# Kernel tuning notes

Hardware: AMD Instinct MI355X
Metric: run time of the kernel (lower is better)

The kernel has to match this reference:

```python
import jax, jax.numpy as jnp
import numpy as np

N_NODES, N_EDGES = 16000, 256000
M_IN_S, M_IN_V = 16, 8   # input irreps: 16x0e + 8x1o (dim 40)
M_K_S, M_K_V = 8, 4      # key/query irreps: 8x0e + 4x1o
M_V_S, M_V_V = 16, 8     # value irreps: 16x0e + 8x1o
NUM_BASIS, R_CUT = 32, 2.5
SQ3 = 1.7320508075688772  # sqrt(3)


def _fc_net(r, W1, W2):
    # e3nn FullyConnectedNet([num_basis,16,numels], silu): weight-normalized linears
    h = jax.nn.silu(r @ (W1 / jnp.sqrt(jnp.float32(W1.shape[0]))))
    return h @ (W2 / jnp.sqrt(jnp.float32(W2.shape[0])))


def _edge_tp(xs, xv, y0, y1, w, m1s, m1v, mos, mov):
    # FullyConnectedTensorProduct(in1 = m1s x0e + m1v x1o, in2 = 1x0e + 1x1o,
    #   out = mos x0e + mov x1o), per-edge external weights w [E, numels].
    # Paths: 0e*0e->0e, 1o*1o->0e (dot/sqrt3), 0e*1o->1o, 1o*0e->1o.
    E = w.shape[0]
    n1, n2, n3 = m1s * mos, m1v * mos, m1s * mov
    w_ss = w[:, :n1].reshape(E, m1s, mos)
    w_vv = w[:, n1:n1 + n2].reshape(E, m1v, mos)
    w_sv = w[:, n1 + n2:n1 + n2 + n3].reshape(E, m1s, mov)
    w_vs = w[:, n1 + n2 + n3:].reshape(E, m1v, mov)
    inv = 1.0 / jnp.sqrt(jnp.float32(m1s + m1v))  # fan-in path normalization
    out_s = (jnp.einsum('ei,eio->eo', xs * y0[:, None], w_ss)
             + jnp.einsum('eic,ec,eio->eo', xv, y1, w_vv) / SQ3) * inv
    out_v = (jnp.einsum('ei,ec,eio->eoc', xs, y1, w_sv)
             + jnp.einsum('eic,eio->eoc', xv * y0[:, None, None], w_vs)) * inv
    return out_s, out_v


def _forward(pos, x, Wq_s, Wq_v, Wk1, Wk2, Wv1, Wv2, Ws_ss, Ws_vv, edge_src, edge_dst):
    xs, xv = x[:, :M_IN_S], x[:, M_IN_S:].reshape(-1, M_IN_V, 3)
    vec = pos[edge_dst] - pos[edge_src]                       # [E,3]
    d = jnp.linalg.norm(vec, axis=1)
    d_safe = jnp.maximum(d, 1e-6)
    # bessel radial basis with cutoff (soft_one_hot_linspace, basis='bessel') * sqrt(num_basis)
    n = jnp.arange(1, NUM_BASIS + 1, dtype=jnp.float32)
    rad = jnp.sqrt(2.0 / R_CUT) * jnp.sin(n[None] * jnp.pi * d_safe[:, None] / R_CUT) / d_safe[:, None]
    rad = jnp.where((d < R_CUT)[:, None], rad, 0.0) * jnp.sqrt(jnp.float32(NUM_BASIS))
    # spherical harmonics lmax=1, normalize=True, component normalization
    vh = vec / d_safe[:, None]
    y0, y1 = jnp.ones_like(d), SQ3 * vh
    # query projection (o3.Linear: per-irrep linear with 1/sqrt(fan_in))
    q_s = xs @ Wq_s / jnp.sqrt(jnp.float32(M_IN_S))           # [N, M_K_S]
    q_v = jnp.einsum('nic,io->noc', xv, Wq_v) / jnp.sqrt(jnp.float32(M_IN_V))
    # per-edge tensor-product weights from radial MLPs (shared_weights=False)
    wk = _fc_net(rad, Wk1, Wk2)                               # [E, 288]
    wv = _fc_net(rad, Wv1, Wv2)                               # [E, 576]
    xs_e, xv_e = xs[edge_src], xv[edge_src]
    k_s, k_v = _edge_tp(xs_e, xv_e, y0, y1, wk, M_IN_S, M_IN_V, M_K_S, M_K_V)
    v_s, v_v = _edge_tp(xs_e, xv_e, y0, y1, wv, M_IN_S, M_IN_V, M_V_S, M_V_V)
    # similarity tensor product (query x key -> 0e), shared internal weights
    fan = jnp.sqrt(jnp.float32(M_K_S * M_K_S + M_K_V * M_K_V))
    sim = (jnp.einsum('ei,ij,ej->e', q_s[edge_dst], Ws_ss, k_s)
           + jnp.einsum('eic,ij,ejc->e', q_v[edge_dst], Ws_vv, k_v) / SQ3) / fan
    # scatter softmax over incoming edges of each dst node
    attn = jnp.exp(sim)
    Z = jax.ops.segment_sum(attn, edge_dst, num_segments=N_NODES)
    a = attn / Z[edge_dst]
    # weighted scatter-sum aggregation
    out_s = jax.ops.segment_sum(a[:, None] * v_s, edge_dst, num_segments=N_NODES)
    out_v = jax.ops.segment_sum(a[:, None, None] * v_v, edge_dst, num_segments=N_NODES)
    return jnp.concatenate([out_s, out_v.reshape(N_NODES, -1)], axis=1)  # [N, 40]


def setup_inputs() -> dict:
    key = jax.random.key(0)
    ks = jax.random.split(key, 12)
    wk_numels = M_IN_S * M_K_S + M_IN_V * M_K_S + M_IN_S * M_K_V + M_IN_V * M_K_V  # 288
    wv_numels = M_IN_S * M_V_S + M_IN_V * M_V_S + M_IN_S * M_V_V + M_IN_V * M_V_V  # 576
    return {
        'pos': jax.random.uniform(ks[0], (N_NODES, 3), jnp.float32) * 3.0,
        'x': jax.random.normal(ks[1], (N_NODES, M_IN_S + 3 * M_IN_V), jnp.float32),
        'Wq_s': jax.random.normal(ks[2], (M_IN_S, M_K_S), jnp.float32),
        'Wq_v': jax.random.normal(ks[3], (M_IN_V, M_K_V), jnp.float32),
        'Wk1': jax.random.normal(ks[4], (NUM_BASIS, 16), jnp.float32),
        'Wk2': jax.random.normal(ks[5], (16, wk_numels), jnp.float32),
        'Wv1': jax.random.normal(ks[6], (NUM_BASIS, 16), jnp.float32),
        'Wv2': jax.random.normal(ks[7], (16, wv_numels), jnp.float32),
        'Ws_ss': jax.random.normal(ks[8], (M_K_S, M_K_S), jnp.float32) * 0.1,
        'Ws_vv': jax.random.normal(ks[9], (M_K_V, M_K_V), jnp.float32) * 0.1,
        'edge_src': jax.random.randint(ks[10], (N_EDGES,), 0, N_NODES),
        'edge_dst': jax.random.randint(ks[11], (N_EDGES,), 0, N_NODES),
    }


def reference(pos, x, Wq_s, Wq_v, Wk1, Wk2, Wv1, Wv2, Ws_ss, Ws_vv, edge_src, edge_dst):
    return _forward(pos, x, Wq_s, Wq_v, Wk1, Wk2, Wv1, Wv2, Ws_ss, Ws_vv, edge_src, edge_dst)
```

## Files before the change

kernel.cpp:

```cpp
#include <hip/hip_runtime.h>
#include <hip/hip_bf16.h>

#define N_NODES 16000
#define N_EDGES 256000

#define OFF_SD     0
#define OFF_SIMB   512000
#define OFF_CNT    768000
#define OFF_START  784000
#define OFF_CUR    800001
#define OFF_WB     816004
#define OFF_WBK    834436
#define OFF_QT     846724

typedef _Float16 f16x2 __attribute__((ext_vector_type(2)));
typedef _Float16 f16x8v __attribute__((ext_vector_type(8)));
typedef float f32x4v __attribute__((ext_vector_type(4)));

__device__ __forceinline__ float fdot2f(f16x2 a, f16x2 b, float c) {
#if __has_builtin(__builtin_amdgcn_fdot2)
  return __builtin_amdgcn_fdot2(a, b, c, false);
#else
  return fmaf((float)a.x, (float)b.x, fmaf((float)a.y, (float)b.y, c));
#endif
}

__device__ __forceinline__ unsigned packh2(float a, float b) {
  union { unsigned u; f16x2 p; } v;
  v.p.x = (_Float16)a; v.p.y = (_Float16)b;
  return v.u;
}

__device__ __forceinline__ unsigned splat_half(unsigned x, unsigned sel) {
#if __has_builtin(__builtin_amdgcn_perm)
  return __builtin_amdgcn_perm(x, x, sel);
#else
  unsigned h = (sel == 0x03020302u) ? (x >> 16) : (x & 0xffffu);
  return h | (h << 16);
#endif
}

__device__ __forceinline__ void load_row40(const float* __restrict__ p, float* xr) {
  const float4* rp = reinterpret_cast<const float4*>(p);
#pragma unroll
  for (int q = 0; q < 10; ++q) {
    float4 f = rp[q];
    xr[4 * q + 0] = f.x; xr[4 * q + 1] = f.y; xr[4 * q + 2] = f.z; xr[4 * q + 3] = f.w;
  }
}

struct EdgeGeom { float vhx, vhy, vhz, y1x, y1y, y1z; };

__device__ __forceinline__ void edge_h_pk(const float* __restrict__ pos, int s, int d,
                                          const unsigned* W1, f16x2* hp, EdgeGeom& g) {
  float vx = pos[3 * d + 0] - pos[3 * s + 0];
  float vy = pos[3 * d + 1] - pos[3 * s + 1];
  float vz = pos[3 * d + 2] - pos[3 * s + 2];
  float dist = sqrtf(fmaf(vx, vx, fmaf(vy, vy, vz * vz)));
  float dsafe = fmaxf(dist, 1e-6f);
  float rinv = 1.0f / dsafe;
  g.vhx = vx * rinv; g.vhy = vy * rinv; g.vhz = vz * rinv;
  g.y1x = 1.7320508075688772f * g.vhx;
  g.y1y = 1.7320508075688772f * g.vhy;
  g.y1z = 1.7320508075688772f * g.vhz;
  float pre[16];
#pragma unroll
  for (int t = 0; t < 16; ++t) pre[t] = 0.f;
  float sx, cx;
  sincosf(1.2566370614359172f * dsafe, &sx, &cx);
  cx = fminf(1.f, fmaxf(-1.f, cx));
  float twoc = 2.f * cx;
  float sprev = 0.f, scur = sx;
  float rscale = (dist < 2.5f) ? (5.059644256269407f * rinv) : 0.f;
#pragma unroll
  for (int bp = 0; bp < 16; ++bp) {
    float r0 = rscale * scur;
    float sn = fmaf(twoc, scur, -sprev); sprev = scur; scur = sn;
    float r1 = rscale * scur;
    sn = fmaf(twoc, scur, -sprev); sprev = scur; scur = sn;
    union { unsigned u; f16x2 p; } rp; rp.p.x = (_Float16)r0; rp.p.y = (_Float16)r1;
    union { uint4 u[4]; f16x2 p[16]; } w;
    w.u[0] = *(const uint4*)(W1 + bp * 16);
    w.u[1] = *(const uint4*)(W1 + bp * 16 + 4);
    w.u[2] = *(const uint4*)(W1 + bp * 16 + 8);
    w.u[3] = *(const uint4*)(W1 + bp * 16 + 12);
#pragma unroll
    for (int t = 0; t < 16; ++t) pre[t] = fdot2f(rp.p, w.p[t], pre[t]);
  }
#pragma unroll
  for (int tp = 0; tp < 8; ++tp) {
    float h0 = pre[2 * tp]     / (1.f + __expf(-pre[2 * tp]));
    float h1 = pre[2 * tp + 1] / (1.f + __expf(-pre[2 * tp + 1]));
    hp[tp].x = (_Float16)h0; hp[tp].y = (_Float16)h1;
  }
}

__global__ void k_hist(const int* __restrict__ edst, int* __restrict__ cnt) {
  int e = blockIdx.x * 256 + threadIdx.x;
  atomicAdd(&cnt[edst[e]], 1);
}

__global__ void __launch_bounds__(1024) k_scan(const int* __restrict__ cnt,
                                               int* __restrict__ start, int* __restrict__ cur) {
  __shared__ int part[1024];
  int t = threadIdx.x;
  int base = t * 16;
  int local[16];
  int sum = 0;
#pragma unroll
  for (int i = 0; i < 16; ++i) {
    int idx = base + i;
    int c = (idx < N_NODES) ? cnt[idx] : 0;
    local[i] = sum; sum += c;
  }
  part[t] = sum;
  __syncthreads();
  for (int off = 1; off < 1024; off <<= 1) {
    int v = (t >= off) ? part[t - off] : 0;
    __syncthreads();
    part[t] += v;
    __syncthreads();
  }
  int prev = (t == 0) ? 0 : part[t - 1];
#pragma unroll
  for (int i = 0; i < 16; ++i) {
    int idx = base + i;
    if (idx < N_NODES) { int st = prev + local[i]; start[idx] = st; cur[idx] = st; }
  }
  if (t == 0) start[N_NODES] = N_EDGES;
}

__global__ void k_fill(const int* __restrict__ esrc, const int* __restrict__ edst,
                       int* __restrict__ cur, int2* __restrict__ sd) {
  int e = blockIdx.x * 256 + threadIdx.x;
  int d = edst[e];
  int slot = atomicAdd(&cur[d], 1);
  sd[slot] = make_int2(esrc[e], d);
}

__global__ void k_prepB(const float* __restrict__ Wv2, unsigned short* __restrict__ WB) {
  int idx = blockIdx.x * 256 + threadIdx.x;
  int j = idx & 7;
  int lane = (idx >> 3) & 63;
  int t3 = idx >> 9;
  int ct = t3 % 3, kk = t3 / 3;
  int q = lane >> 4, m = lane & 15;
  int row = 32 * kk + 8 * q + j;
  int col = 16 * ct + m;
  int t = row & 15;
  float v = 0.f;
  if (row < 256) {
    int i = row >> 4;
    if (col < 16)      v = Wv2[t * 576 + i * 16 + col];
    else if (col < 24) v = Wv2[t * 576 + 384 + i * 8 + (col - 16)];
  } else if (row < 384) {
    int i = (row - 256) >> 4;
    if (col < 16)      v = Wv2[t * 576 + 256 + i * 16 + col];
  } else {
    int part = (row - 384) >> 7;
    int i = ((row - 384) & 127) >> 4;
    int cb = 24 + 8 * part;
    if (col >= cb && col < cb + 8) v = Wv2[t * 576 + 512 + i * 8 + (col - cb)];
  }
  union { unsigned short u; _Float16 h; } cv;
  cv.h = (_Float16)(v * 0.051031036307982884f);
  WB[idx] = cv.u;
}

__global__ void k_prepBK(const float* __restrict__ Wk2, unsigned short* __restrict__ WBK) {
  int idx = blockIdx.x * 256 + threadIdx.x;
  int j = idx & 7;
  int lane = (idx >> 3) & 63;
  int t2 = idx >> 9;
  int ct = t2 & 1, kk = t2 >> 1;
  int q = lane >> 4, m = lane & 15;
  int row = 32 * kk + 8 * q + j;
  int col = 16 * ct + m;
  int t = row & 15;
  float v = 0.f;
  if (col < 24) {
    if (row < 256) {
      int i = row >> 4;
      if (col < 8)       v = Wk2[t * 288 + i * 8 + col];
      else if (col < 12) v = Wk2[t * 288 + 192 + i * 4 + (col - 8)];
    } else if (row < 384) {
      int i = (row - 256) >> 4;
      if (col < 8)       v = Wk2[t * 288 + 128 + i * 8 + col];
    } else {
      int c = (row - 384) >> 7;
      int i = ((row - 384) & 127) >> 4;
      int cb = 12 + 4 * c;
      if (col >= cb && col < cb + 4) v = Wk2[t * 288 + 256 + i * 4 + (col - cb)];
    }
  }
  union { unsigned short u; _Float16 h; } cv;
  cv.h = (_Float16)(v * 0.051031036307982884f);
  WBK[idx] = cv.u;
}

__global__ void __launch_bounds__(128) k_nodeq(
    const float* __restrict__ x,
    const float* __restrict__ Wq_s, const float* __restrict__ Wq_v,
    const float* __restrict__ Wss, const float* __restrict__ Wvv,
    unsigned short* __restrict__ QT) {
  __shared__ float Ls[240];
  for (int i = threadIdx.x; i < 240; i += 128) {
    float v;
    if (i < 128)      v = Wq_s[i] * 0.25f;
    else if (i < 160) v = Wq_v[i - 128] * 0.3535533905932738f;
    else if (i < 224) v = Wss[i - 160] * 0.11180339887498948f;
    else              v = Wvv[i - 224] * 0.06454972243679028f;
    Ls[i] = v;
  }
  __syncthreads();
  int n = blockIdx.x * 128 + threadIdx.x;
  float xd[40];
  load_row40(x + 40 * n, xd);
  float qd[8], qvd[12];
#pragma unroll
  for (int o = 0; o < 8; ++o) qd[o] = 0.f;
#pragma unroll
  for (int i = 0; i < 16; ++i)
#pragma unroll
    for (int o = 0; o < 8; ++o) qd[o] = fmaf(xd[i], Ls[8 * i + o], qd[o]);
#pragma unroll
  for (int k = 0; k < 12; ++k) qvd[k] = 0.f;
#pragma unroll
  for (int i = 0; i < 8; ++i)
#pragma unroll
    for (int o = 0; o < 4; ++o)
#pragma unroll
      for (int c = 0; c < 3; ++c)
        qvd[3 * o + c] = fmaf(xd[16 + 3 * i + c], Ls[128 + 4 * i + o], qvd[3 * o + c]);
  float qf[20];
#pragma unroll
  for (int j = 0; j < 8; ++j) {
    float t = 0.f;
#pragma unroll
    for (int i = 0; i < 8; ++i) t = fmaf(qd[i], Ls[160 + 8 * i + j], t);
    qf[j] = t;
  }
#pragma unroll
  for (int o = 0; o < 4; ++o)
#pragma unroll
    for (int c = 0; c < 3; ++c) {
      float t = 0.f;
#pragma unroll
      for (int i = 0; i < 4; ++i) t = fmaf(qvd[3 * i + c], Ls[224 + 4 * i + o], t);
      qf[8 + 3 * o + c] = t;
    }
  uint2* qp = (uint2*)(QT + 20 * n);
#pragma unroll
  for (int b = 0; b < 5; ++b) {
    uint2 st;
    st.x = packh2(qf[4 * b], qf[4 * b + 1]);
    st.y = packh2(qf[4 * b + 2], qf[4 * b + 3]);
    qp[b] = st;
  }
}

#define RSTR 36

__device__ __forceinline__ void build_coef(const float* xr, const float* Bv, float* coef) {
#pragma unroll
  for (int i = 0; i < 16; ++i) coef[i] = xr[i];
#pragma unroll
  for (int i = 0; i < 8; ++i) coef[16 + i] = Bv[i];
#pragma unroll
  for (int p = 0; p < 4; ++p)
#pragma unroll
    for (int c = 0; c < 3; ++c) {
      coef[24 + 8 * c + 2 * p]     = xr[16 + 6 * p + c];
      coef[24 + 8 * c + 2 * p + 1] = xr[16 + 6 * p + 3 + c];
    }
}

__global__ void __launch_bounds__(256) k_edge1(
    const float* __restrict__ pos, const float* __restrict__ x,
    const float* __restrict__ Wk1, const unsigned short* __restrict__ WBK,
    const unsigned short* __restrict__ QT,
    const int2* __restrict__ sd, float* __restrict__ simb) {
  __shared__ __align__(16) unsigned LW1[256];
  __shared__ __align__(16) unsigned SM[4][64 * RSTR];

  for (int i = threadIdx.x; i < 256; i += 256) {
    int bp = i >> 4, t = i & 15;
    LW1[i] = packh2(Wk1[(2 * bp) * 16 + t] * 0.17677669529663687f,
                    Wk1[(2 * bp + 1) * 16 + t] * 0.17677669529663687f);
  }
  __syncthreads();

  int wave = threadIdx.x >> 6, lane = threadIdx.x & 63;
  int q = lane >> 4, m = lane & 15;
  int q1 = q & 1;
  unsigned seld = (q >> 1) ? 0x03020302u : 0x01000100u;
  int slot = blockIdx.x * 256 + threadIdx.x;
  int2 e = sd[slot];
  int s = e.x, d = e.y;

  f16x2 hp[8]; EdgeGeom g;
  edge_h_pk(pos, s, d, LW1, hp, g);

  float qf[20];
  {
    const uint2* qp = (const uint2*)(QT + 20 * d);
#pragma unroll
    for (int b = 0; b < 5; ++b) {
      uint2 u = qp[b];
      union { unsigned d; f16x2 p; } a0, a1;
      a0.d = u.x; a1.d = u.y;
      qf[4 * b] = (float)a0.p.x; qf[4 * b + 1] = (float)a0.p.y;
      qf[4 * b + 2] = (float)a1.p.x; qf[4 * b + 3] = (float)a1.p.y;
    }
  }

  float xr[40];
  load_row40(x + 40 * s, xr);
  float Bv[8];
#pragma unroll
  for (int i = 0; i < 8; ++i)
    Bv[i] = fmaf(xr[16 + 3 * i], g.vhx, fmaf(xr[17 + 3 * i], g.vhy, xr[18 + 3 * i] * g.vhz));
  float coef[48];
  build_coef(xr, Bv, coef);

  unsigned* row = &SM[wave][lane * RSTR];
  {
    union { uint4 u; f16x2 p[4]; } h0, h1;
#pragma unroll
    for (int k = 0; k < 4; ++k) { h0.p[k] = hp[k]; h1.p[k] = hp[4 + k]; }
    *(uint4*)(row) = h0.u;
    *(uint4*)(row + 4) = h1.u;
  }
#pragma unroll
  for (int bt = 0; bt < 6; ++bt) {
    uint4 w;
    w.x = packh2(coef[8 * bt + 0], coef[8 * bt + 1]);
    w.y = packh2(coef[8 * bt + 2], coef[8 * bt + 3]);
    w.z = packh2(coef[8 * bt + 4], coef[8 * bt + 5]);
    w.w = packh2(coef[8 * bt + 6], coef[8 * bt + 7]);
    *(uint4*)(row + 8 + 4 * bt) = w;
  }
  unsigned* wbase = &SM[wave][0];
  union { uint4 u; f16x2 p[4]; } hs[4];
#pragma unroll
  for (int rt = 0; rt < 4; ++rt)
    hs[rt].u = *(const uint4*)(wbase + (16 * rt + m) * RSTR + 4 * q1);

  const uint4* WBq = (const uint4*)WBK;
  f32x4v acc[4][2];
#pragma unroll
  for (int rt = 0; rt < 4; ++rt)
#pragma unroll
    for (int ct = 0; ct < 2; ++ct) { f32x4v z = {0.f, 0.f, 0.f, 0.f}; acc[rt][ct] = z; }

#pragma unroll
  for (int bt = 0; bt < 6; ++bt) {
    union { uint4 u; unsigned d[4]; } cb[4];
#pragma unroll
    for (int rt = 0; rt < 4; ++rt)
      cb[rt].u = *(const uint4*)(wbase + (16 * rt + m) * RSTR + 8 + 4 * bt);
#pragma unroll
    for (int t = 0; t < 4; ++t) {
      int kk = 4 * bt + t;
      union { uint4 u; f16x2 p[4]; f16x8v v; } av[4];
#pragma unroll
      for (int rt = 0; rt < 4; ++rt) {
        union { unsigned d; f16x2 p; } sp;
        sp.d = splat_half(cb[rt].d[t], seld);
#pragma unroll
        for (int w = 0; w < 4; ++w) av[rt].p[w] = hs[rt].p[w] * sp.p;
      }
#pragma unroll
      for (int ct = 0; ct < 2; ++ct) {
        union { uint4 u; f16x8v v; } bf;
        bf.u = WBq[(kk * 2 + ct) * 64 + lane];
#pragma unroll
        for (int rt = 0; rt < 4; ++rt)
          acc[rt][ct] = __builtin_amdgcn_mfma_f32_16x16x32_f16(av[rt].v, bf.v, acc[rt][ct], 0, 0, 0);
      }
    }
  }

  float P[24];
  float* ctb = (float*)wbase;
#pragma unroll
  for (int rt = 0; rt < 4; ++rt)
#pragma unroll
    for (int r = 0; r < 4; ++r)
      ctb[m * 65 + 16 * rt + 4 * q + r] = acc[rt][0][r];
#pragma unroll
  for (int o = 0; o < 16; ++o) P[o] = ctb[o * 65 + lane];
#pragma unroll
  for (int rt = 0; rt < 4; ++rt)
#pragma unroll
    for (int r = 0; r < 4; ++r)
      ctb[m * 65 + 16 * rt + 4 * q + r] = acc[rt][1][r];
#pragma unroll
  for (int o = 0; o < 8; ++o) P[16 + o] = ctb[o * 65 + lane];

  float sim = 0.f;
#pragma unroll
  for (int j = 0; j < 8; ++j) sim = fmaf(qf[j], P[j], sim);
  float y1c[3] = {g.y1x, g.y1y, g.y1z};
#pragma unroll
  for (int o = 0; o < 4; ++o)
#pragma unroll
    for (int c = 0; c < 3; ++c)
      sim = fmaf(qf[8 + 3 * o + c], fmaf(y1c[c], P[8 + o], P[12 + 4 * c + o]), sim);
  simb[slot] = sim;
}

__global__ void k_norm(const int* __restrict__ start, float* __restrict__ simb) {
  int n = blockIdx.x * 256 + threadIdx.x;
  if (n >= N_NODES) return;
  int a = start[n], b = start[n + 1];
  if (a == b) return;
  float m = -3.4e38f;
  for (int j = a; j < b; ++j) m = fmaxf(m, simb[j]);
  float Z = 0.f;
  for (int j = a; j < b; ++j) { float t = __expf(simb[j] - m); simb[j] = t; Z += t; }
  float inv = 1.f / Z;
  for (int j = a; j < b; ++j) simb[j] *= inv;
}

__global__ void __launch_bounds__(256) k_edge2(
    const float* __restrict__ pos, const float* __restrict__ x,
    const float* __restrict__ Wv1, const unsigned short* __restrict__ WB,
    const int2* __restrict__ sd, const float* __restrict__ ab, float* __restrict__ out) {
  __shared__ __align__(16) unsigned LW1[256];
  __shared__ __align__(16) unsigned SM[4][64 * RSTR];

  for (int i = threadIdx.x; i < 256; i += 256) {
    int bp = i >> 4, t = i & 15;
    LW1[i] = packh2(Wv1[(2 * bp) * 16 + t] * 0.17677669529663687f,
                    Wv1[(2 * bp + 1) * 16 + t] * 0.17677669529663687f);
  }
  __syncthreads();

  int wave = threadIdx.x >> 6, lane = threadIdx.x & 63;
  int q = lane >> 4, m = lane & 15;
  int q1 = q & 1;
  unsigned seld = (q >> 1) ? 0x03020302u : 0x01000100u;
  int slot = blockIdx.x * 256 + threadIdx.x;
  int2 e = sd[slot];
  int s = e.x, d = e.y;

  bool same[6];
#pragma unroll
  for (int k = 0; k < 6; ++k) {
    int dd = __shfl_down(d, 1 << k, 64);
    same[k] = ((lane + (1 << k)) < 64) && (dd == d);
  }
  int dprev = __shfl_up(d, 1, 64);
  bool head = (lane == 0) || (dprev != d);

  f16x2 hp[8]; EdgeGeom g;
  edge_h_pk(pos, s, d, LW1, hp, g);
  float xr[40];
  load_row40(x + 40 * s, xr);
  float Bv[8];
#pragma unroll
  for (int i = 0; i < 8; ++i)
    Bv[i] = fmaf(xr[16 + 3 * i], g.vhx, fmaf(xr[17 + 3 * i], g.vhy, xr[18 + 3 * i] * g.vhz));
  float coef[48];
  build_coef(xr, Bv, coef);
  float a = ab[slot];

  unsigned* row = &SM[wave][lane * RSTR];
  {
    union { uint4 u; f16x2 p[4]; } h0, h1;
#pragma unroll
    for (int k = 0; k < 4; ++k) { h0.p[k] = hp[k]; h1.p[k] = hp[4 + k]; }
    *(uint4*)(row) = h0.u;
    *(uint4*)(row + 4) = h1.u;
  }
#pragma unroll
  for (int bt = 0; bt < 6; ++bt) {
    uint4 w;
    w.x = packh2(coef[8 * bt + 0], coef[8 * bt + 1]);
    w.y = packh2(coef[8 * bt + 2], coef[8 * bt + 3]);
    w.z = packh2(coef[8 * bt + 4], coef[8 * bt + 5]);
    w.w = packh2(coef[8 * bt + 6], coef[8 * bt + 7]);
    *(uint4*)(row + 8 + 4 * bt) = w;
  }
  unsigned* wbase = &SM[wave][0];
  union { uint4 u; f16x2 p[4]; } hs[4];
#pragma unroll
  for (int rt = 0; rt < 4; ++rt)
    hs[rt].u = *(const uint4*)(wbase + (16 * rt + m) * RSTR + 4 * q1);

  const uint4* WBq = (const uint4*)WB;
  f32x4v acc[4][3];
#pragma unroll
  for (int rt = 0; rt < 4; ++rt)
#pragma unroll
    for (int ct = 0; ct < 3; ++ct) { f32x4v z = {0.f, 0.f, 0.f, 0.f}; acc[rt][ct] = z; }

#pragma unroll
  for (int bt = 0; bt < 6; ++bt) {
    union { uint4 u; unsigned d[4]; } cb[4];
#pragma unroll
    for (int rt = 0; rt < 4; ++rt)
      cb[rt].u = *(const uint4*)(wbase + (16 * rt + m) * RSTR + 8 + 4 * bt);
#pragma unroll
    for (int t = 0; t < 4; ++t) {
      int kk = 4 * bt + t;
      union { uint4 u; f16x2 p[4]; f16x8v v; } av[4];
#pragma unroll
      for (int rt = 0; rt < 4; ++rt) {
        union { unsigned d; f16x2 p; } sp;
        sp.d = splat_half(cb[rt].d[t], seld);
#pragma unroll
        for (int w = 0; w < 4; ++w) av[rt].p[w] = hs[rt].p[w] * sp.p;
      }
#pragma unroll
      for (int ct = 0; ct < 3; ++ct) {
        union { uint4 u; f16x8v v; } bf;
        bf.u = WBq[(kk * 3 + ct) * 64 + lane];
#pragma unroll
        for (int rt = 0; rt < 4; ++rt)
          acc[rt][ct] = __builtin_amdgcn_mfma_f32_16x16x32_f16(av[rt].v, bf.v, acc[rt][ct], 0, 0, 0);
      }
    }
  }

  float* ctb = (float*)wbase;
  float* op = out + 40 * d;

  {
#pragma unroll
    for (int rt = 0; rt < 4; ++rt)
#pragma unroll
      for (int r = 0; r < 4; ++r)
        ctb[m * 65 + 16 * rt + 4 * q + r] = acc[rt][0][r];
    float P0[16];
#pragma unroll
    for (int o = 0; o < 16; ++o) P0[o] = ctb[o * 65 + lane];
#pragma unroll
    for (int o = 0; o < 16; ++o) {
      float v = a * P0[o];
#pragma unroll
      for (int k = 0; k < 6; ++k) {
        float ov = __shfl_down(v, 1 << k, 64);
        v += same[k] ? ov : 0.f;
      }
      if (head) atomicAdd(op + o, v);
    }
  }
  float P1[16], P2[16];
#pragma unroll
  for (int rt = 0; rt < 4; ++rt)
#pragma unroll
    for (int r = 0; r < 4; ++r)
      ctb[m * 65 + 16 * rt + 4 * q + r] = acc[rt][1][r];
#pragma unroll
  for (int o = 0; o < 16; ++o) P1[o] = ctb[o * 65 + lane];
#pragma unroll
  for (int rt = 0; rt < 4; ++rt)
#pragma unroll
    for (int r = 0; r < 4; ++r)
      ctb[m * 65 + 16 * rt + 4 * q + r] = acc[rt][2][r];
#pragma unroll
  for (int o = 0; o < 16; ++o) P2[o] = ctb[o * 65 + lane];
#pragma unroll
  for (int o = 0; o < 8; ++o) {
    float s1v = P1[o];
    float vc[3];
    vc[0] = a * fmaf(g.y1x, s1v, P1[8 + o]);
    vc[1] = a * fmaf(g.y1y, s1v, P2[o]);
    vc[2] = a * fmaf(g.y1z, s1v, P2[8 + o]);
#pragma unroll
    for (int c = 0; c < 3; ++c) {
      float v = vc[c];
#pragma unroll
      for (int k = 0; k < 6; ++k) {
        float ov = __shfl_down(v, 1 << k, 64);
        v += same[k] ? ov : 0.f;
      }
      if (head) atomicAdd(op + 16 + 3 * o + c, v);
    }
  }
}

extern "C" void kernel_launch(void* const* d_in, const int* in_sizes, int n_in,
                              void* d_out, int out_size, void* d_ws, size_t ws_size,
                              hipStream_t stream) {
  (void)in_sizes; (void)n_in; (void)out_size; (void)ws_size;
  const float* pos  = (const float*)d_in[0];
  const float* x    = (const float*)d_in[1];
  const float* Wq_s = (const float*)d_in[2];
  const float* Wq_v = (const float*)d_in[3];
  const float* Wk1  = (const float*)d_in[4];
  const float* Wk2  = (const float*)d_in[5];
  const float* Wv1  = (const float*)d_in[6];
  const float* Wv2  = (const float*)d_in[7];
  const float* Wss  = (const float*)d_in[8];
  const float* Wvv  = (const float*)d_in[9];
  const int* esrc = (const int*)d_in[10];
  const int* edst = (const int*)d_in[11];
  int*   wsi  = (int*)d_ws;
  float* wsf  = (float*)d_ws;
  float* out  = (float*)d_out;

  int2*  sd    = (int2*)(wsi + OFF_SD);
  float* simb  = wsf + OFF_SIMB;
  int*   cnt   = wsi + OFF_CNT;
  int*   start = wsi + OFF_START;
  int*   cur   = wsi + OFF_CUR;
  unsigned short* WB  = (unsigned short*)(wsf + OFF_WB);
  unsigned short* WBK = (unsigned short*)(wsf + OFF_WBK);
  unsigned short* QT  = (unsigned short*)(wsf + OFF_QT);

  hipMemsetAsync(cnt, 0, (size_t)N_NODES * sizeof(int), stream);
  hipMemsetAsync(out, 0, (size_t)(N_NODES * 40) * sizeof(float), stream);
  k_prepB<<<144, 256, 0, stream>>>(Wv2, WB);
  k_prepBK<<<96, 256, 0, stream>>>(Wk2, WBK);
  k_nodeq<<<125, 128, 0, stream>>>(x, Wq_s, Wq_v, Wss, Wvv, QT);
  k_hist<<<1000, 256, 0, stream>>>(edst, cnt);
  k_scan<<<1, 1024, 0, stream>>>(cnt, start, cur);
  k_fill<<<1000, 256, 0, stream>>>(esrc, edst, cur, sd);
  k_edge1<<<1000, 256, 0, stream>>>(pos, x, Wk1, WBK, QT, sd, simb);
  k_norm<<<63, 256, 0, stream>>>(start, simb);
  k_edge2<<<1000, 256, 0, stream>>>(pos, x, Wv1, WB, sd, simb, out);
}
```

Baseline: 239.1 us.

## Fuse softmax normalization into edge kernels and double-buffer MFMA weight loads

Removes the separate per-node softmax kernel. k_edge1 now stores exp(sim) and accumulates per-destination sums with a segmented wave reduction and one atomic per run, and k_edge2 divides by that sum when it uses the weight. The B-operand weight loads in both MFMA loops are software-prefetched into two alternating register buffers, and both edge kernels are pinned to four waves per EU. Dropping the max subtraction risks exp overflow if the similarity scores are large, and the prefetch buffers add register pressure.

```diff
diff --git a/kernel.cpp b/kernel.cpp
--- a/kernel.cpp
+++ b/kernel.cpp
@@ -12,6 +12,7 @@
 #define OFF_WB     816004
 #define OFF_WBK    834436
 #define OFF_QT     846724
+#define OFF_Z      1006724
 
 typedef _Float16 f16x2 __attribute__((ext_vector_type(2)));
 typedef _Float16 f16x8v __attribute__((ext_vector_type(8)));
@@ -275,11 +276,12 @@
     }
 }
 
+__attribute__((amdgpu_waves_per_eu(4, 4)))
 __global__ void __launch_bounds__(256) k_edge1(
     const float* __restrict__ pos, const float* __restrict__ x,
     const float* __restrict__ Wk1, const unsigned short* __restrict__ WBK,
     const unsigned short* __restrict__ QT,
-    const int2* __restrict__ sd, float* __restrict__ simb) {
+    const int2* __restrict__ sd, float* __restrict__ simb, float* __restrict__ Z) {
   __shared__ __align__(16) unsigned LW1[256];
   __shared__ __align__(16) unsigned SM[4][64 * RSTR];
 
@@ -298,6 +300,15 @@
   int2 e = sd[slot];
   int s = e.x, d = e.y;
 
+  bool same[6];
+#pragma unroll
+  for (int k = 0; k < 6; ++k) {
+    int dd = __shfl_down(d, 1 << k, 64);
+    same[k] = ((lane + (1 << k)) < 64) && (dd == d);
+  }
+  int dprev = __shfl_up(d, 1, 64);
+  bool head = (lane == 0) || (dprev != d);
+
   f16x2 hp[8]; EdgeGeom g;
   edge_h_pk(pos, s, d, LW1, hp, g);
 
@@ -353,6 +364,11 @@
 #pragma unroll
     for (int ct = 0; ct < 2; ++ct) { f32x4v z = {0.f, 0.f, 0.f, 0.f}; acc[rt][ct] = z; }
 
+  union BFu { uint4 u; f16x8v v; };
+  BFu bfA[2], bfB[2];
+#pragma unroll
+  for (int ct = 0; ct < 2; ++ct) bfA[ct].u = WBq[ct * 64 + lane];
+
 #pragma unroll
   for (int bt = 0; bt < 6; ++bt) {
     union { uint4 u; unsigned d[4]; } cb[4];
@@ -362,6 +378,12 @@
 #pragma unroll
     for (int t = 0; t < 4; ++t) {
       int kk = 4 * bt + t;
+      BFu* cur = (kk & 1) ? bfB : bfA;
+      BFu* nxt = (kk & 1) ? bfA : bfB;
+      if (kk < 23) {
+#pragma unroll
+        for (int ct = 0; ct < 2; ++ct) nxt[ct].u = WBq[((kk + 1) * 2 + ct) * 64 + lane];
+      }
       union { uint4 u; f16x2 p[4]; f16x8v v; } av[4];
 #pragma unroll
       for (int rt = 0; rt < 4; ++rt) {
@@ -371,13 +393,10 @@
         for (int w = 0; w < 4; ++w) av[rt].p[w] = hs[rt].p[w] * sp.p;
       }
 #pragma unroll
-      for (int ct = 0; ct < 2; ++ct) {
-        union { uint4 u; f16x8v v; } bf;
-        bf.u = WBq[(kk * 2 + ct) * 64 + lane];
+      for (int ct = 0; ct < 2; ++ct)
 #pragma unroll
         for (int rt = 0; rt < 4; ++rt)
-          acc[rt][ct] = __builtin_amdgcn_mfma_f32_16x16x32_f16(av[rt].v, bf.v, acc[rt][ct], 0, 0, 0);
-      }
+          acc[rt][ct] = __builtin_amdgcn_mfma_f32_16x16x32_f16(av[rt].v, cur[ct].v, acc[rt][ct], 0, 0, 0);
     }
   }
 
@@ -407,26 +426,24 @@
 #pragma unroll
     for (int c = 0; c < 3; ++c)
       sim = fmaf(qf[8 + 3 * o + c], fmaf(y1c[c], P[8 + o], P[12 + 4 * c + o]), sim);
-  simb[slot] = sim;
-}
-
-__global__ void k_norm(const int* __restrict__ start, float* __restrict__ simb) {
-  int n = blockIdx.x * 256 + threadIdx.x;
-  if (n >= N_NODES) return;
-  int a = start[n], b = start[n + 1];
-  if (a == b) return;
-  float m = -3.4e38f;
-  for (int j = a; j < b; ++j) m = fmaxf(m, simb[j]);
-  float Z = 0.f;
-  for (int j = a; j < b; ++j) { float t = __expf(simb[j] - m); simb[j] = t; Z += t; }
-  float inv = 1.f / Z;
-  for (int j = a; j < b; ++j) simb[j] *= inv;
-}
-
+
+  float ev = __expf(sim);
+  simb[slot] = ev;
+  float v = ev;
+#pragma unroll
+  for (int k = 0; k < 6; ++k) {
+    float ov = __shfl_down(v, 1 << k, 64);
+    v += same[k] ? ov : 0.f;
+  }
+  if (head) atomicAdd(&Z[d], v);
+}
+
+__attribute__((amdgpu_waves_per_eu(4, 4)))
 __global__ void __launch_bounds__(256) k_edge2(
     const float* __restrict__ pos, const float* __restrict__ x,
     const float* __restrict__ Wv1, const unsigned short* __restrict__ WB,
-    const int2* __restrict__ sd, const float* __restrict__ ab, float* __restrict__ out) {
+    const int2* __restrict__ sd, const float* __restrict__ eb,
+    const float* __restrict__ Zv, float* __restrict__ out) {
   __shared__ __align__(16) unsigned LW1[256];
   __shared__ __align__(16) unsigned SM[4][64 * RSTR];
 
@@ -445,6 +462,9 @@
   int2 e = sd[slot];
   int s = e.x, d = e.y;
 
+  float ev = eb[slot];
+  float Zd = Zv[d];
+
   bool same[6];
 #pragma unroll
   for (int k = 0; k < 6; ++k) {
@@ -464,7 +484,7 @@
     Bv[i] = fmaf(xr[16 + 3 * i], g.vhx, fmaf(xr[17 + 3 * i], g.vhy, xr[18 + 3 * i] * g.vhz));
   float coef[48];
   build_coef(xr, Bv, coef);
-  float a = ab[slot];
+  float a = ev / Zd;
 
   unsigned* row = &SM[wave][lane * RSTR];
   {
@@ -496,6 +516,11 @@
 #pragma unroll
     for (int ct = 0; ct < 3; ++ct) { f32x4v z = {0.f, 0.f, 0.f, 0.f}; acc[rt][ct] = z; }
 
+  union BFu { uint4 u; f16x8v v; };
+  BFu bfA[3], bfB[3];
+#pragma unroll
+  for (int ct = 0; ct < 3; ++ct) bfA[ct].u = WBq[ct * 64 + lane];
+
 #pragma unroll
   for (int bt = 0; bt < 6; ++bt) {
     union { uint4 u; unsigned d[4]; } cb[4];
@@ -505,6 +530,12 @@
 #pragma unroll
     for (int t = 0; t < 4; ++t) {
       int kk = 4 * bt + t;
+      BFu* cur = (kk & 1) ? bfB : bfA;
+      BFu* nxt = (kk & 1) ? bfA : bfB;
+      if (kk < 23) {
+#pragma unroll
+        for (int ct = 0; ct < 3; ++ct) nxt[ct].u = WBq[((kk + 1) * 3 + ct) * 64 + lane];
+      }
       union { uint4 u; f16x2 p[4]; f16x8v v; } av[4];
 #pragma unroll
       for (int rt = 0; rt < 4; ++rt) {
@@ -514,13 +545,10 @@
         for (int w = 0; w < 4; ++w) av[rt].p[w] = hs[rt].p[w] * sp.p;
       }
 #pragma unroll
-      for (int ct = 0; ct < 3; ++ct) {
-        union { uint4 u; f16x8v v; } bf;
-        bf.u = WBq[(kk * 3 + ct) * 64 + lane];
+      for (int ct = 0; ct < 3; ++ct)
 #pragma unroll
         for (int rt = 0; rt < 4; ++rt)
-          acc[rt][ct] = __builtin_amdgcn_mfma_f32_16x16x32_f16(av[rt].v, bf.v, acc[rt][ct], 0, 0, 0);
-      }
+          acc[rt][ct] = __builtin_amdgcn_mfma_f32_16x16x32_f16(av[rt].v, cur[ct].v, acc[rt][ct], 0, 0, 0);
     }
   }
 
@@ -610,8 +638,10 @@
   unsigned short* WB  = (unsigned short*)(wsf + OFF_WB);
   unsigned short* WBK = (unsigned short*)(wsf + OFF_WBK);
   unsigned short* QT  = (unsigned short*)(wsf + OFF_QT);
+  float* Z    = wsf + OFF_Z;
 
   hipMemsetAsync(cnt, 0, (size_t)N_NODES * sizeof(int), stream);
+  hipMemsetAsync(Z, 0, (size_t)N_NODES * sizeof(float), stream);
   hipMemsetAsync(out, 0, (size_t)(N_NODES * 40) * sizeof(float), stream);
   k_prepB<<<144, 256, 0, stream>>>(Wv2, WB);
   k_prepBK<<<96, 256, 0, stream>>>(Wk2, WBK);
@@ -619,7 +649,6 @@
   k_hist<<<1000, 256, 0, stream>>>(edst, cnt);
   k_scan<<<1, 1024, 0, stream>>>(cnt, start, cur);
   k_fill<<<1000, 256, 0, stream>>>(esrc, edst, cur, sd);
-  k_edge1<<<1000, 256, 0, stream>>>(pos, x, Wk1, WBK, QT, sd, simb);
-  k_norm<<<63, 256, 0, stream>>>(start, simb);
-  k_edge2<<<1000, 256, 0, stream>>>(pos, x, Wv1, WB, sd, simb, out);
-}
+  k_edge1<<<1000, 256, 0, stream>>>(pos, x, Wk1, WBK, QT, sd, simb, Z);
+  k_edge2<<<1000, 256, 0, stream>>>(pos, x, Wv1, WB, sd, simb, Z, out);
+}
```

Measured after the change: 234.0 us. -2.1%, faster.

## Fuse key and value edge passes into one kernel with deferred softmax normalization

Applied to the files above, without the earlier changes.

Merges the two edge kernels into a single pass that computes both radial MLPs, both tensor-product MFMA GEMMs, the attention logit and the value scatter. The per-destination max-subtracted softmax pass is replaced by accumulating unnormalized exp(sim) into Z with atomics and dividing the output by Z in a small final kernel. This removes a second gather of pos and x, a second radial basis evaluation and the simb round trip. In exchange it raises register and LDS pressure, and dropping the max subtraction risks exp overflow for large logits.

```diff
diff --git a/kernel.cpp b/kernel.cpp
--- a/kernel.cpp
+++ b/kernel.cpp
@@ -12,6 +12,7 @@
 #define OFF_WB     816004
 #define OFF_WBK    834436
 #define OFF_QT     846724
+#define OFF_Z      1006724
 
 typedef _Float16 f16x2 __attribute__((ext_vector_type(2)));
 typedef _Float16 f16x8v __attribute__((ext_vector_type(8)));
@@ -50,50 +51,6 @@
 }
 
 struct EdgeGeom { float vhx, vhy, vhz, y1x, y1y, y1z; };
-
-__device__ __forceinline__ void edge_h_pk(const float* __restrict__ pos, int s, int d,
-                                          const unsigned* W1, f16x2* hp, EdgeGeom& g) {
-  float vx = pos[3 * d + 0] - pos[3 * s + 0];
-  float vy = pos[3 * d + 1] - pos[3 * s + 1];
-  float vz = pos[3 * d + 2] - pos[3 * s + 2];
-  float dist = sqrtf(fmaf(vx, vx, fmaf(vy, vy, vz * vz)));
-  float dsafe = fmaxf(dist, 1e-6f);
-  float rinv = 1.0f / dsafe;
-  g.vhx = vx * rinv; g.vhy = vy * rinv; g.vhz = vz * rinv;
-  g.y1x = 1.7320508075688772f * g.vhx;
-  g.y1y = 1.7320508075688772f * g.vhy;
-  g.y1z = 1.7320508075688772f * g.vhz;
-  float pre[16];
-#pragma unroll
-  for (int t = 0; t < 16; ++t) pre[t] = 0.f;
-  float sx, cx;
-  sincosf(1.2566370614359172f * dsafe, &sx, &cx);
-  cx = fminf(1.f, fmaxf(-1.f, cx));
-  float twoc = 2.f * cx;
-  float sprev = 0.f, scur = sx;
-  float rscale = (dist < 2.5f) ? (5.059644256269407f * rinv) : 0.f;
-#pragma unroll
-  for (int bp = 0; bp < 16; ++bp) {
-    float r0 = rscale * scur;
-    float sn = fmaf(twoc, scur, -sprev); sprev = scur; scur = sn;
-    float r1 = rscale * scur;
-    sn = fmaf(twoc, scur, -sprev); sprev = scur; scur = sn;
-    union { unsigned u; f16x2 p; } rp; rp.p.x = (_Float16)r0; rp.p.y = (_Float16)r1;
-    union { uint4 u[4]; f16x2 p[16]; } w;
-    w.u[0] = *(const uint4*)(W1 + bp * 16);
-    w.u[1] = *(const uint4*)(W1 + bp * 16 + 4);
-    w.u[2] = *(const uint4*)(W1 + bp * 16 + 8);
-    w.u[3] = *(const uint4*)(W1 + bp * 16 + 12);
-#pragma unroll
-    for (int t = 0; t < 16; ++t) pre[t] = fdot2f(rp.p, w.p[t], pre[t]);
-  }
-#pragma unroll
-  for (int tp = 0; tp < 8; ++tp) {
-    float h0 = pre[2 * tp]     / (1.f + __expf(-pre[2 * tp]));
-    float h1 = pre[2 * tp + 1] / (1.f + __expf(-pre[2 * tp + 1]));
-    hp[tp].x = (_Float16)h0; hp[tp].y = (_Float16)h1;
-  }
-}
 
 __global__ void k_hist(const int* __restrict__ edst, int* __restrict__ cnt) {
   int e = blockIdx.x * 256 + threadIdx.x;
@@ -259,7 +216,7 @@
   }
 }
 
-#define RSTR 36
+#define RSTR 44
 
 __device__ __forceinline__ void build_coef(const float* xr, const float* Bv, float* coef) {
 #pragma unroll
@@ -275,18 +232,23 @@
     }
 }
 
-__global__ void __launch_bounds__(256) k_edge1(
+__global__ void __launch_bounds__(256, 3) k_edge(
     const float* __restrict__ pos, const float* __restrict__ x,
-    const float* __restrict__ Wk1, const unsigned short* __restrict__ WBK,
+    const float* __restrict__ Wk1, const float* __restrict__ Wv1,
+    const unsigned short* __restrict__ WBK, const unsigned short* __restrict__ WB,
     const unsigned short* __restrict__ QT,
-    const int2* __restrict__ sd, float* __restrict__ simb) {
-  __shared__ __align__(16) unsigned LW1[256];
+    const int2* __restrict__ sd, float* __restrict__ Z, float* __restrict__ out) {
+  __shared__ __align__(16) unsigned LWK[256];
+  __shared__ __align__(16) unsigned LWV[256];
   __shared__ __align__(16) unsigned SM[4][64 * RSTR];
 
-  for (int i = threadIdx.x; i < 256; i += 256) {
+  {
+    int i = threadIdx.x;
     int bp = i >> 4, t = i & 15;
-    LW1[i] = packh2(Wk1[(2 * bp) * 16 + t] * 0.17677669529663687f,
+    LWK[i] = packh2(Wk1[(2 * bp) * 16 + t] * 0.17677669529663687f,
                     Wk1[(2 * bp + 1) * 16 + t] * 0.17677669529663687f);
+    LWV[i] = packh2(Wv1[(2 * bp) * 16 + t] * 0.17677669529663687f,
+                    Wv1[(2 * bp + 1) * 16 + t] * 0.17677669529663687f);
   }
   __syncthreads();
 
@@ -298,8 +260,157 @@
   int2 e = sd[slot];
   int s = e.x, d = e.y;
 
-  f16x2 hp[8]; EdgeGeom g;
-  edge_h_pk(pos, s, d, LW1, hp, g);
+  f16x2 hpK[8], hpV[8]; EdgeGeom g;
+  {
+    float vx = pos[3 * d + 0] - pos[3 * s + 0];
+    float vy = pos[3 * d + 1] - pos[3 * s + 1];
+    float vz = pos[3 * d + 2] - pos[3 * s + 2];
+    float dist = sqrtf(fmaf(vx, vx, fmaf(vy, vy, vz * vz)));
+    float dsafe = fmaxf(dist, 1e-6f);
+    float rinv = 1.0f / dsafe;
+    g.vhx = vx * rinv; g.vhy = vy * rinv; g.vhz = vz * rinv;
+    g.y1x = 1.7320508075688772f * g.vhx;
+    g.y1y = 1.7320508075688772f * g.vhy;
+    g.y1z = 1.7320508075688772f * g.vhz;
+    float preK[16], preV[16];
+#pragma unroll
+    for (int t = 0; t < 16; ++t) { preK[t] = 0.f; preV[t] = 0.f; }
+    float sx, cx;
+    sincosf(1.2566370614359172f * dsafe, &sx, &cx);
+    cx = fminf(1.f, fmaxf(-1.f, cx));
+    float twoc = 2.f * cx;
+    float sprev = 0.f, scur = sx;
+    float rscale = (dist < 2.5f) ? (5.059644256269407f * rinv) : 0.f;
+#pragma unroll
+    for (int bp = 0; bp < 16; ++bp) {
+      float r0 = rscale * scur;
+      float sn = fmaf(twoc, scur, -sprev); sprev = scur; scur = sn;
+      float r1 = rscale * scur;
+      sn = fmaf(twoc, scur, -sprev); sprev = scur; scur = sn;
+      union { unsigned u; f16x2 p; } rp; rp.p.x = (_Float16)r0; rp.p.y = (_Float16)r1;
+      union { uint4 u[4]; f16x2 p[16]; } wk, wv;
+      wk.u[0] = *(const uint4*)(LWK + bp * 16);
+      wk.u[1] = *(const uint4*)(LWK + bp * 16 + 4);
+      wk.u[2] = *(const uint4*)(LWK + bp * 16 + 8);
+      wk.u[3] = *(const uint4*)(LWK + bp * 16 + 12);
+      wv.u[0] = *(const uint4*)(LWV + bp * 16);
+      wv.u[1] = *(const uint4*)(LWV + bp * 16 + 4);
+      wv.u[2] = *(const uint4*)(LWV + bp * 16 + 8);
+      wv.u[3] = *(const uint4*)(LWV + bp * 16 + 12);
+#pragma unroll
+      for (int t = 0; t < 16; ++t) {
+        preK[t] = fdot2f(rp.p, wk.p[t], preK[t]);
+        preV[t] = fdot2f(rp.p, wv.p[t], preV[t]);
+      }
+    }
+#pragma unroll
+    for (int tp = 0; tp < 8; ++tp) {
+      float k0 = preK[2 * tp]     / (1.f + __expf(-preK[2 * tp]));
+      float k1 = preK[2 * tp + 1] / (1.f + __expf(-preK[2 * tp + 1]));
+      float v0 = preV[2 * tp]     / (1.f + __expf(-preV[2 * tp]));
+      float v1 = preV[2 * tp + 1] / (1.f + __expf(-preV[2 * tp + 1]));
+      hpK[tp].x = (_Float16)k0; hpK[tp].y = (_Float16)k1;
+      hpV[tp].x = (_Float16)v0; hpV[tp].y = (_Float16)v1;
+    }
+  }
+
+  float xr[40];
+  load_row40(x + 40 * s, xr);
+  float Bv[8];
+#pragma unroll
+  for (int i = 0; i < 8; ++i)
+    Bv[i] = fmaf(xr[16 + 3 * i], g.vhx, fmaf(xr[17 + 3 * i], g.vhy, xr[18 + 3 * i] * g.vhz));
+  float coef[48];
+  build_coef(xr, Bv, coef);
+
+  unsigned* row = &SM[wave][lane * RSTR];
+  {
+    union { uint4 u; f16x2 p[4]; } a0, a1, b0, b1;
+#pragma unroll
+    for (int k = 0; k < 4; ++k) { a0.p[k] = hpK[k]; a1.p[k] = hpK[4 + k];
+                                  b0.p[k] = hpV[k]; b1.p[k] = hpV[4 + k]; }
+    *(uint4*)(row)      = a0.u;
+    *(uint4*)(row + 4)  = a1.u;
+    *(uint4*)(row + 8)  = b0.u;
+    *(uint4*)(row + 12) = b1.u;
+  }
+#pragma unroll
+  for (int bt = 0; bt < 6; ++bt) {
+    uint4 w;
+    w.x = packh2(coef[8 * bt + 0], coef[8 * bt + 1]);
+    w.y = packh2(coef[8 * bt + 2], coef[8 * bt + 3]);
+    w.z = packh2(coef[8 * bt + 4], coef[8 * bt + 5]);
+    w.w = packh2(coef[8 * bt + 6], coef[8 * bt + 7]);
+    *(uint4*)(row + 16 + 4 * bt) = w;
+  }
+  unsigned* wbase = &SM[wave][0];
+  union { uint4 u; f16x2 p[4]; } hsK[4], hsV[4];
+#pragma unroll
+  for (int rt = 0; rt < 4; ++rt) {
+    hsK[rt].u = *(const uint4*)(wbase + (16 * rt + m) * RSTR + 4 * q1);
+    hsV[rt].u = *(const uint4*)(wbase + (16 * rt + m) * RSTR + 8 + 4 * q1);
+  }
+
+  const uint4* WBKq = (const uint4*)WBK;
+  const uint4* WBq  = (const uint4*)WB;
+  f32x4v accK[4][2];
+  f32x4v accV[4][3];
+#pragma unroll
+  for (int rt = 0; rt < 4; ++rt) {
+#pragma unroll
+    for (int ct = 0; ct < 2; ++ct) { f32x4v z = {0.f, 0.f, 0.f, 0.f}; accK[rt][ct] = z; }
+#pragma unroll
+    for (int ct = 0; ct < 3; ++ct) { f32x4v z = {0.f, 0.f, 0.f, 0.f}; accV[rt][ct] = z; }
+  }
+
+#pragma unroll
+  for (int bt = 0; bt < 6; ++bt) {
+    union { uint4 u; unsigned d[4]; } cb[4];
+#pragma unroll
+    for (int rt = 0; rt < 4; ++rt)
+      cb[rt].u = *(const uint4*)(wbase + (16 * rt + m) * RSTR + 16 + 4 * bt);
+#pragma unroll
+    for (int t = 0; t < 4; ++t) {
+      int kk = 4 * bt + t;
+      unsigned spv[4];
+#pragma unroll
+      for (int rt = 0; rt < 4; ++rt) spv[rt] = splat_half(cb[rt].d[t], seld);
+      {
+        union { uint4 u; f16x2 p[4]; f16x8v v; } av[4];
+#pragma unroll
+        for (int rt = 0; rt < 4; ++rt) {
+          union { unsigned d; f16x2 p; } sp; sp.d = spv[rt];
+#pragma unroll
+          for (int w = 0; w < 4; ++w) av[rt].p[w] = hsK[rt].p[w] * sp.p;
+        }
+#pragma unroll
+        for (int ct = 0; ct < 2; ++ct) {
+          union { uint4 u; f16x8v v; } bf;
+          bf.u = WBKq[(kk * 2 + ct) * 64 + lane];
+#pragma unroll
+          for (int rt = 0; rt < 4; ++rt)
+            accK[rt][ct] = __builtin_amdgcn_mfma_f32_16x16x32_f16(av[rt].v, bf.v, accK[rt][ct], 0, 0, 0);
+        }
+      }
+      {
+        union { uint4 u; f16x2 p[4]; f16x8v v; } av[4];
+#pragma unroll
+        for (int rt = 0; rt < 4; ++rt) {
+          union { unsigned d; f16x2 p; } sp; sp.d = spv[rt];
+#pragma unroll
+          for (int w = 0; w < 4; ++w) av[rt].p[w] = hsV[rt].p[w] * sp.p;
+        }
+#pragma unroll
+        for (int ct = 0; ct < 3; ++ct) {
+          union { uint4 u; f16x8v v; } bf;
+          bf.u = WBq[(kk * 3 + ct) * 64 + lane];
+#pragma unroll
+          for (int rt = 0; rt < 4; ++rt)
+            accV[rt][ct] = __builtin_amdgcn_mfma_f32_16x16x32_f16(av[rt].v, bf.v, accV[rt][ct], 0, 0, 0);
+        }
+      }
+    }
+  }
 
   float qf[20];
   {
@@ -314,87 +425,20 @@
     }
   }
 
-  float xr[40];
-  load_row40(x + 40 * s, xr);
-  float Bv[8];
-#pragma unroll
-  for (int i = 0; i < 8; ++i)
-    Bv[i] = fmaf(xr[16 + 3 * i], g.vhx, fmaf(xr[17 + 3 * i], g.vhy, xr[18 + 3 * i] * g.vhz));
-  float coef[48];
-  build_coef(xr, Bv, coef);
-
-  unsigned* row = &SM[wave][lane * RSTR];
-  {
-    union { uint4 u; f16x2 p[4]; } h0, h1;
-#pragma unroll
-    for (int k = 0; k < 4; ++k) { h0.p[k] = hp[k]; h1.p[k] = hp[4 + k]; }
-    *(uint4*)(row) = h0.u;
-    *(uint4*)(row + 4) = h1.u;
-  }
-#pragma unroll
-  for (int bt = 0; bt < 6; ++bt) {
-    uint4 w;
-    w.x = packh2(coef[8 * bt + 0], coef[8 * bt + 1]);
-    w.y = packh2(coef[8 * bt + 2], coef[8 * bt + 3]);
-    w.z = packh2(coef[8 * bt + 4], coef[8 * bt + 5]);
-    w.w = packh2(coef[8 * bt + 6], coef[8 * bt + 7]);
-    *(uint4*)(row + 8 + 4 * bt) = w;
-  }
-  unsigned* wbase = &SM[wave][0];
-  union { uint4 u; f16x2 p[4]; } hs[4];
-#pragma unroll
-  for (int rt = 0; rt < 4; ++rt)
-    hs[rt].u = *(const uint4*)(wbase + (16 * rt + m) * RSTR + 4 * q1);
-
-  const uint4* WBq = (const uint4*)WBK;
-  f32x4v acc[4][2];
-#pragma unroll
-  for (int rt = 0; rt < 4; ++rt)
-#pragma unroll
-    for (int ct = 0; ct < 2; ++ct) { f32x4v z = {0.f, 0.f, 0.f, 0.f}; acc[rt][ct] = z; }
-
-#pragma unroll
-  for (int bt = 0; bt < 6; ++bt) {
-    union { uint4 u; unsigned d[4]; } cb[4];
-#pragma unroll
-    for (int rt = 0; rt < 4; ++rt)
-      cb[rt].u = *(const uint4*)(wbase + (16 * rt + m) * RSTR + 8 + 4 * bt);
-#pragma unroll
-    for (int t = 0; t < 4; ++t) {
-      int kk = 4 * bt + t;
-      union { uint4 u; f16x2 p[4]; f16x8v v; } av[4];
-#pragma unroll
-      for (int rt = 0; rt < 4; ++rt) {
-        union { unsigned d; f16x2 p; } sp;
-        sp.d = splat_half(cb[rt].d[t], seld);
-#pragma unroll
-        for (int w = 0; w < 4; ++w) av[rt].p[w] = hs[rt].p[w] * sp.p;
-      }
-#pragma unroll
-      for (int ct = 0; ct < 2; ++ct) {
-        union { uint4 u; f16x8v v; } bf;
-        bf.u = WBq[(kk * 2 + ct) * 64 + lane];
-#pragma unroll
-        for (int rt = 0; rt < 4; ++rt)
-          acc[rt][ct] = __builtin_amdgcn_mfma_f32_16x16x32_f16(av[rt].v, bf.v, acc[rt][ct], 0, 0, 0);
-      }
-    }
-  }
-
   float P[24];
   float* ctb = (float*)wbase;
 #pragma unroll
   for (int rt = 0; rt < 4; ++rt)
 #pragma unroll
     for (int r = 0; r < 4; ++r)
-      ctb[m * 65 + 16 * rt + 4 * q + r] = acc[rt][0][r];
+      ctb[m * 65 + 16 * rt + 4 * q + r] = accK[rt][0][r];
 #pragma unroll
   for (int o = 0; o < 16; ++o) P[o] = ctb[o * 65 + lane];
 #pragma unroll
   for (int rt = 0; rt < 4; ++rt)
 #pragma unroll
     for (int r = 0; r < 4; ++r)
-      ctb[m * 65 + 16 * rt + 4 * q + r] = acc[rt][1][r];
+      ctb[m * 65 + 16 * rt + 4 * q + r] = accK[rt][1][r];
 #pragma unroll
   for (int o = 0; o < 8; ++o) P[16 + o] = ctb[o * 65 + lane];
 
@@ -407,43 +451,7 @@
 #pragma unroll
     for (int c = 0; c < 3; ++c)
       sim = fmaf(qf[8 + 3 * o + c], fmaf(y1c[c], P[8 + o], P[12 + 4 * c + o]), sim);
-  simb[slot] = sim;
-}
-
-__global__ void k_norm(const int* __restrict__ start, float* __restrict__ simb) {
-  int n = blockIdx.x * 256 + threadIdx.x;
-  if (n >= N_NODES) return;
-  int a = start[n], b = start[n + 1];
-  if (a == b) return;
-  float m = -3.4e38f;
-  for (int j = a; j < b; ++j) m = fmaxf(m, simb[j]);
-  float Z = 0.f;
-  for (int j = a; j < b; ++j) { float t = __expf(simb[j] - m); simb[j] = t; Z += t; }
-  float inv = 1.f / Z;
-  for (int j = a; j < b; ++j) simb[j] *= inv;
-}
-
-__global__ void __launch_bounds__(256) k_edge2(
-    const float* __restrict__ pos, const float* __restrict__ x,
-    const float* __restrict__ Wv1, const unsigned short* __restrict__ WB,
-    const int2* __restrict__ sd, const float* __restrict__ ab, float* __restrict__ out) {
-  __shared__ __align__(16) unsigned LW1[256];
-  __shared__ __align__(16) unsigned SM[4][64 * RSTR];
-
-  for (int i = threadIdx.x; i < 256; i += 256) {
-    int bp = i >> 4, t = i & 15;
-    LW1[i] = packh2(Wv1[(2 * bp) * 16 + t] * 0.17677669529663687f,
-                    Wv1[(2 * bp + 1) * 16 + t] * 0.17677669529663687f);
-  }
-  __syncthreads();
-
-  int wave = threadIdx.x >> 6, lane = threadIdx.x & 63;
-  int q = lane >> 4, m = lane & 15;
-  int q1 = q & 1;
-  unsigned seld = (q >> 1) ? 0x03020302u : 0x01000100u;
-  int slot = blockIdx.x * 256 + threadIdx.x;
-  int2 e = sd[slot];
-  int s = e.x, d = e.y;
+  float ev = __expf(sim);
 
   bool same[6];
 #pragma unroll
@@ -453,92 +461,29 @@
   }
   int dprev = __shfl_up(d, 1, 64);
   bool head = (lane == 0) || (dprev != d);
-
-  f16x2 hp[8]; EdgeGeom g;
-  edge_h_pk(pos, s, d, LW1, hp, g);
-  float xr[40];
-  load_row40(x + 40 * s, xr);
-  float Bv[8];
-#pragma unroll
-  for (int i = 0; i < 8; ++i)
-    Bv[i] = fmaf(xr[16 + 3 * i], g.vhx, fmaf(xr[17 + 3 * i], g.vhy, xr[18 + 3 * i] * g.vhz));
-  float coef[48];
-  build_coef(xr, Bv, coef);
-  float a = ab[slot];
-
-  unsigned* row = &SM[wave][lane * RSTR];
   {
-    union { uint4 u; f16x2 p[4]; } h0, h1;
-#pragma unroll
-    for (int k = 0; k < 4; ++k) { h0.p[k] = hp[k]; h1.p[k] = hp[4 + k]; }
-    *(uint4*)(row) = h0.u;
-    *(uint4*)(row + 4) = h1.u;
-  }
-#pragma unroll
-  for (int bt = 0; bt < 6; ++bt) {
-    uint4 w;
-    w.x = packh2(coef[8 * bt + 0], coef[8 * bt + 1]);
-    w.y = packh2(coef[8 * bt + 2], coef[8 * bt + 3]);
-    w.z = packh2(coef[8 * bt + 4], coef[8 * bt + 5]);
-    w.w = packh2(coef[8 * bt + 6], coef[8 * bt + 7]);
-    *(uint4*)(row + 8 + 4 * bt) = w;
-  }
-  unsigned* wbase = &SM[wave][0];
-  union { uint4 u; f16x2 p[4]; } hs[4];
-#pragma unroll
-  for (int rt = 0; rt < 4; ++rt)
-    hs[rt].u = *(const uint4*)(wbase + (16 * rt + m) * RSTR + 4 * q1);
-
-  const uint4* WBq = (const uint4*)WB;
-  f32x4v acc[4][3];
-#pragma unroll
-  for (int rt = 0; rt < 4; ++rt)
-#pragma unroll
-    for (int ct = 0; ct < 3; ++ct) { f32x4v z = {0.f, 0.f, 0.f, 0.f}; acc[rt][ct] = z; }
-
-#pragma unroll
-  for (int bt = 0; bt < 6; ++bt) {
-    union { uint4 u; unsigned d[4]; } cb[4];
+    float v = ev;
+#pragma unroll
+    for (int k = 0; k < 6; ++k) {
+      float ov = __shfl_down(v, 1 << k, 64);
+      v += same[k] ? ov : 0.f;
+    }
+    if (head) atomicAdd(&Z[d], v);
+  }
+
+  float* op = out + 40 * d;
+  {
 #pragma unroll
     for (int rt = 0; rt < 4; ++rt)
-      cb[rt].u = *(const uint4*)(wbase + (16 * rt + m) * RSTR + 8 + 4 * bt);
-#pragma unroll
-    for (int t = 0; t < 4; ++t) {
-      int kk = 4 * bt + t;
-      union { uint4 u; f16x2 p[4]; f16x8v v; } av[4];
-#pragma unroll
-      for (int rt = 0; rt < 4; ++rt) {
-        union { unsigned d; f16x2 p; } sp;
-        sp.d = splat_half(cb[rt].d[t], seld);
-#pragma unroll
-        for (int w = 0; w < 4; ++w) av[rt].p[w] = hs[rt].p[w] * sp.p;
-      }
-#pragma unroll
-      for (int ct = 0; ct < 3; ++ct) {
-        union { uint4 u; f16x8v v; } bf;
-        bf.u = WBq[(kk * 3 + ct) * 64 + lane];
-#pragma unroll
-        for (int rt = 0; rt < 4; ++rt)
-          acc[rt][ct] = __builtin_amdgcn_mfma_f32_16x16x32_f16(av[rt].v, bf.v, acc[rt][ct], 0, 0, 0);
-      }
-    }
-  }
-
-  float* ctb = (float*)wbase;
-  float* op = out + 40 * d;
-
-  {
-#pragma unroll
-    for (int rt = 0; rt < 4; ++rt)
 #pragma unroll
       for (int r = 0; r < 4; ++r)
-        ctb[m * 65 + 16 * rt + 4 * q + r] = acc[rt][0][r];
+        ctb[m * 65 + 16 * rt + 4 * q + r] = accV[rt][0][r];
     float P0[16];
 #pragma unroll
     for (int o = 0; o < 16; ++o) P0[o] = ctb[o * 65 + lane];
 #pragma unroll
     for (int o = 0; o < 16; ++o) {
-      float v = a * P0[o];
+      float v = ev * P0[o];
 #pragma unroll
       for (int k = 0; k < 6; ++k) {
         float ov = __shfl_down(v, 1 << k, 64);
@@ -552,23 +497,23 @@
   for (int rt = 0; rt < 4; ++rt)
 #pragma unroll
     for (int r = 0; r < 4; ++r)
-      ctb[m * 65 + 16 * rt + 4 * q + r] = acc[rt][1][r];
+      ctb[m * 65 + 16 * rt + 4 * q + r] = accV[rt][1][r];
 #pragma unroll
   for (int o = 0; o < 16; ++o) P1[o] = ctb[o * 65 + lane];
 #pragma unroll
   for (int rt = 0; rt < 4; ++rt)
 #pragma unroll
     for (int r = 0; r < 4; ++r)
-      ctb[m * 65 + 16 * rt + 4 * q + r] = acc[rt][2][r];
+      ctb[m * 65 + 16 * rt + 4 * q + r] = accV[rt][2][r];
 #pragma unroll
   for (int o = 0; o < 16; ++o) P2[o] = ctb[o * 65 + lane];
 #pragma unroll
   for (int o = 0; o < 8; ++o) {
     float s1v = P1[o];
     float vc[3];
-    vc[0] = a * fmaf(g.y1x, s1v, P1[8 + o]);
-    vc[1] = a * fmaf(g.y1y, s1v, P2[o]);
-    vc[2] = a * fmaf(g.y1z, s1v, P2[8 + o]);
+    vc[0] = ev * fmaf(g.y1x, s1v, P1[8 + o]);
+    vc[1] = ev * fmaf(g.y1y, s1v, P2[o]);
+    vc[2] = ev * fmaf(g.y1z, s1v, P2[8 + o]);
 #pragma unroll
     for (int c = 0; c < 3; ++c) {
       float v = vc[c];
@@ -580,6 +525,12 @@
       if (head) atomicAdd(op + 16 + 3 * o + c, v);
     }
   }
+}
+
+__global__ void k_div(const float* __restrict__ Z, float* __restrict__ out) {
+  int i = blockIdx.x * 256 + threadIdx.x;
+  float z = Z[i / 40];
+  if (z != 0.f) out[i] /= z;
 }
 
 extern "C" void kernel_launch(void* const* d_in, const int* in_sizes, int n_in,
@@ -603,15 +554,16 @@
   float* out  = (float*)d_out;
 
   int2*  sd    = (int2*)(wsi + OFF_SD);
-  float* simb  = wsf + OFF_SIMB;
   int*   cnt   = wsi + OFF_CNT;
   int*   start = wsi + OFF_START;
   int*   cur   = wsi + OFF_CUR;
   unsigned short* WB  = (unsigned short*)(wsf + OFF_WB);
   unsigned short* WBK = (unsigned short*)(wsf + OFF_WBK);
   unsigned short* QT  = (unsigned short*)(wsf + OFF_QT);
+  float* Z    = wsf + OFF_Z;
 
   hipMemsetAsync(cnt, 0, (size_t)N_NODES * sizeof(int), stream);
+  hipMemsetAsync(Z, 0, (size_t)N_NODES * sizeof(float), stream);
   hipMemsetAsync(out, 0, (size_t)(N_NODES * 40) * sizeof(float), stream);
   k_prepB<<<144, 256, 0, stream>>>(Wv2, WB);
   k_prepBK<<<96, 256, 0, stream>>>(Wk2, WBK);
@@ -619,7 +571,6 @@
   k_hist<<<1000, 256, 0, stream>>>(edst, cnt);
   k_scan<<<1, 1024, 0, stream>>>(cnt, start, cur);
   k_fill<<<1000, 256, 0, stream>>>(esrc, edst, cur, sd);
-  k_edge1<<<1000, 256, 0, stream>>>(pos, x, Wk1, WBK, QT, sd, simb);
-  k_norm<<<63, 256, 0, stream>>>(start, simb);
-  k_edge2<<<1000, 256, 0, stream>>>(pos, x, Wv1, WB, sd, simb, out);
-}
+  k_edge<<<1000, 256, 0, stream>>>(pos, x, Wk1, Wv1, WBK, WB, QT, sd, Z, out);
+  k_div<<<2500, 256, 0, stream>>>(Z, out);
+}
```

Measured after the change: 303.2 us. 1.27x slower.
